# Kernel tuning notes

Hardware: AMD Instinct MI355X
Metric: run time of the kernel (lower is better)

## Reference

```python
import jax, jax.numpy as jnp
import numpy as np

NEG_SLOPE = 0.2
NUM_GRAPHS = 64


def _gatv2_layer(x, src, dst, Wl, bl, Wr, br, att, bias, n_nodes, heads, ch):
    # lin_l (source) and lin_r (target) transforms -> [N, H, C]
    xs = (x @ Wl + bl).reshape(n_nodes, heads, ch)
    xd = (x @ Wr + br).reshape(n_nodes, heads, ch)
    s = xs[src]                                   # [E, H, C] gathered source feats
    e = jax.nn.leaky_relu(s + xd[dst], NEG_SLOPE)  # GATv2: leaky_relu BEFORE att dot
    score = jnp.einsum('ehc,hc->eh', e, att)       # [E, H]
    # segment softmax over edges sharing the same target node
    smax = jax.ops.segment_max(score, dst, num_segments=n_nodes)
    ex = jnp.exp(score - smax[dst])
    denom = jax.ops.segment_sum(ex, dst, num_segments=n_nodes)
    alpha = ex / denom[dst]                        # [E, H]
    out = jax.ops.segment_sum(alpha[:, :, None] * s, dst, num_segments=n_nodes)
    return out.reshape(n_nodes, heads * ch) + bias


def setup_inputs() -> dict:
    key = jax.random.key(0)
    ks = jax.random.split(key, 20)
    N, E, F = 50000, 800000, 128
    H, C = 4, 64
    G = NUM_GRAPHS
    sc = 0.05
    inp = {
        'x': jax.random.normal(ks[0], (N, F), jnp.float32),
        'edge_index': jax.random.randint(ks[1], (2, E), 0, N, jnp.int64 if jax.config.read('jax_enable_x64') else jnp.int32).astype(jnp.int32),
        'batch': jnp.sort(jax.random.randint(ks[2], (N,), 0, G)).astype(jnp.int32),
        'W_l1': jax.random.normal(ks[3], (F, H * C)) * sc,
        'b_l1': jax.random.normal(ks[4], (H * C,)) * sc,
        'W_r1': jax.random.normal(ks[5], (F, H * C)) * sc,
        'b_r1': jax.random.normal(ks[6], (H * C,)) * sc,
        'att1': jax.random.normal(ks[7], (H, C)) * sc,
        'bias1': jax.random.normal(ks[8], (H * C,)) * sc,
        'W_l2': jax.random.normal(ks[9], (H * C, C)) * sc,
        'b_l2': jax.random.normal(ks[10], (C,)) * sc,
        'W_r2': jax.random.normal(ks[11], (H * C, C)) * sc,
        'b_r2': jax.random.normal(ks[12], (C,)) * sc,
        'att2': jax.random.normal(ks[13], (1, C)) * sc,
        'bias2': jax.random.normal(ks[14], (C,)) * sc,
        'W_lin': jax.random.normal(ks[15], (C, 1)) * sc,
        'b_lin': jax.random.normal(ks[16], (1,)) * sc,
    }
    return inp


def reference(x, edge_index, batch, W_l1, b_l1, W_r1, b_r1, att1, bias1,
              W_l2, b_l2, W_r2, b_r2, att2, bias2, W_lin, b_lin):
    N = x.shape[0]
    # PyG GATv2Conv adds self-loops by default
    loops = jnp.arange(N, dtype=edge_index.dtype)
    src = jnp.concatenate([edge_index[0], loops])
    dst = jnp.concatenate([edge_index[1], loops])

    h = _gatv2_layer(x, src, dst, W_l1, b_l1, W_r1, b_r1, att1, bias1, N, 4, 64)
    h = jax.nn.relu(h)  # dropout=identity (eval), norm=Identity
    h = _gatv2_layer(h, src, dst, W_l2, b_l2, W_r2, b_r2, att2, bias2, N, 1, 64)

    # global mean pool over graphs
    sums = jax.ops.segment_sum(h, batch, num_segments=NUM_GRAPHS)
    counts = jax.ops.segment_sum(jnp.ones((N,), h.dtype), batch, num_segments=NUM_GRAPHS)
    pooled = sums / jnp.maximum(counts, 1.0)[:, None]  # [G, 64]
    return pooled @ W_lin + b_lin                      # [G, 1]
```

## Files before the change

kernel.cpp:

```cpp
#include <hip/hip_runtime.h>
#include <hip/hip_bf16.h>
#include <math.h>

typedef __attribute__((ext_vector_type(8))) short short8;
typedef __attribute__((ext_vector_type(4))) float floatx4;
typedef __attribute__((ext_vector_type(2))) float f32x2;

#define ATT_SCALE 0.865617024533378f
#define C_ABS 0.6666666666667f
#define PCLAMP 86.5f

__device__ __forceinline__ float bf2f(unsigned short u) {
  union { unsigned int i; float f; } v; v.i = ((unsigned int)u) << 16; return v.f;
}
__device__ __forceinline__ unsigned short f2bf(float f) {
  union { float f; unsigned int u; } v; v.f = f;
  unsigned int r = (v.u + 0x7fffu + ((v.u >> 16) & 1u)) >> 16;
  return (unsigned short)r;
}
__device__ __forceinline__ int imin(int a, int b) { return a < b ? a : b; }
__device__ __forceinline__ int iclamp(int v, int lo, int hi) {
  return v < lo ? lo : (v > hi ? hi : v);
}
__device__ __forceinline__ float uasf(unsigned int u) {
// ... 142 lines not shown
  }
  if (i < N) {
    int ex = sm[tid] - v + boff;
    rowptr[i] = ex;
    cursor[i] = ex;
    if (i == N - 1) rowptr[N] = ex + v;
  }
}

template <int K, int CT, int RT>
__device__ __forceinline__ void gemm2r_body(
    int bx, int by, int tid,
    const unsigned short* __restrict__ A,
    const unsigned short* __restrict__ BTl, const unsigned short* __restrict__ BTr,
    const unsigned short* __restrict__ bl, const unsigned short* __restrict__ br,
    unsigned short* __restrict__ outl, unsigned short* __restrict__ outr,
    int Nrows, int M) {
  constexpr int KI = K / 32;
  int lane = tid & 63;
  int wave = tid >> 6;
  int r = lane & 15, q = lane >> 4;
  int col0 = by * (4 * CT * 16) + wave * (CT * 16);
  int row0 = bx * (16 * RT);
  short8 Bl[KI][CT], Br[KI][CT];
#pragma unroll
  for (int t = 0; t < CT; ++t) {
    const unsigned short* bpl = BTl + (size_t)(col0 + t * 16 + r) * K + q * 8;
    const unsigned short* bpr = BTr + (size_t)(col0 + t * 16 + r) * K + q * 8;
#pragma unroll
    for (int k = 0; k < KI; ++k) {
      Bl[k][t] = *reinterpret_cast<const short8*>(bpl + k * 32);
      Br[k][t] = *reinterpret_cast<const short8*>(bpr + k * 32);
    }
  }
  float bvl[CT], bvr[CT];
#pragma unroll
  for (int t = 0; t < CT; ++t) {
    bvl[t] = bf2f(bl[col0 + t * 16 + r]);
    bvr[t] = bf2f(br[col0 + t * 16 + r]);
  }
  short8 a[KI], an[KI];
  {
    int ar0 = imin(row0 + r, Nrows - 1);
    const unsigned short* Ap = A + (size_t)ar0 * K + q * 8;
#pragma unroll
    for (int k = 0; k < KI; ++k) a[k] = *reinterpret_cast<const short8*>(Ap + k * 32);
  }
  for (int rt = 0; rt < RT; ++rt) {
    if (rt + 1 < RT) {
      int arn = imin(row0 + (rt + 1) * 16 + r, Nrows - 1);
      const unsigned short* Apn = A + (size_t)arn * K + q * 8;
#pragma unroll
      for (int k = 0; k < KI; ++k) an[k] = *reinterpret_cast<const short8*>(Apn + k * 32);
    }
    floatx4 accl[CT], accr[CT];
#pragma unroll
    for (int t = 0; t < CT; ++t) {
      accl[t] = (floatx4){0.f, 0.f, 0.f, 0.f};
      accr[t] = (floatx4){0.f, 0.f, 0.f, 0.f};
    }
#pragma unroll
    for (int k = 0; k < KI; ++k) {
#pragma unroll
      for (int t = 0; t < CT; ++t) {
        accl[t] = __builtin_amdgcn_mfma_f32_16x16x32_bf16(a[k], Bl[k][t], accl[t], 0, 0, 0);
        accr[t] = __builtin_amdgcn_mfma_f32_16x16x32_bf16(a[k], Br[k][t], accr[t], 0, 0, 0);
      }
    }
#pragma unroll
    for (int t = 0; t < CT; ++t) {
      int col = col0 + t * 16 + r;
#pragma unroll
      for (int rr = 0; rr < 4; ++rr) {
        int row = row0 + rt * 16 + q * 4 + rr;
        if (row < Nrows) {
          outl[(size_t)row * M + col] = f2bf(accl[t][rr] + bvl[t]);
          outr[(size_t)row * M + col] = f2bf(accr[t][rr] + bvr[t]);
        }
      }
    }
#pragma unroll
    for (int k = 0; k < KI; ++k) a[k] = an[k];
  }
}

__global__ __launch_bounds__(256) void k_phase1(
    const unsigned short* __restrict__ A0, const unsigned short* __restrict__ A1,
    const int* __restrict__ dflag,
    const unsigned short* __restrict__ BTl, const unsigned short* __restrict__ BTr,
    const unsigned short* __restrict__ bl, const unsigned short* __restrict__ br,
    unsigned short* __restrict__ outl, unsigned short* __restrict__ outr,
    int Nrows, int M, int nG, int nS,
    const int* __restrict__ esrc, const int* __restrict__ edst,
    const int* __restrict__ rowptr, int* cursor, int* colx, int E, int N) {
  int b = blockIdx.x;
  int m2 = 2 * imin(nG, nS);
  bool isG;
  int idx;
  if (b < m2) { isG = (b & 1) == 0; idx = b >> 1; }
  else        { isG = nG > nS;      idx = imin(nG, nS) + (b - m2); }
  if (isG) {
    const unsigned short* A = dflag[0] ? A1 : A0;
    gemm2r_body<128, 2, 8>(idx >> 1, idx & 1, threadIdx.x, A, BTl, BTr, bl, br,
                           outl, outr, Nrows, M);
    return;
  }
  int ET = E + N;
  int base = idx * 1024 + threadIdx.x;
#pragma unroll
  for (int k = 0; k < 4; ++k) {
    int e = base + k * 256;
    if (e < ET) {
      if (e < E) {
        int s = iclamp(esrc[e], 0, N - 1), d = iclamp(edst[e], 0, N - 1);
        int pos = atomicAdd(&cursor[d], 1);
        colx[iclamp(pos, 0, ET - 1)] = s;
      } else {
        int i = e - E;
        colx[rowptr[i + 1] - 1] = i;
      }
    }
  }
}

__global__ __launch_bounds__(256) void k_gemm2r_l2(
    const unsigned short* __restrict__ A,
    const unsigned short* __restrict__ BTl, const unsigned short* __restrict__ BTr,
    const unsigned short* __restrict__ bl, const unsigned short* __restrict__ br,
    unsigned short* __restrict__ outl, unsigned short* __restrict__ outr,
    int Nrows, int M) {
  gemm2r_body<256, 1, 4>(blockIdx.x, 0, threadIdx.x, A, BTl, BTr, bl, br,
                         outl, outr, Nrows, M);
}

#define EDGE_P(U, V01, V23, P)                                                \
  V01 = (f32x2){uasf(U.x << 16), uasf(U.x & 0xffff0000u)};                    \
  V23 = (f32x2){uasf(U.y << 16), uasf(U.y & 0xffff0000u)};                    \
  {                                                                           \
    f32x2 q01 = a01 * V01 + ad01;                                             \
    f32x2 q23 = a23 * V23 + ad23;                                             \
    f32x2 t01 = c01 * absv2(q01) + q01;                                       \
    f32x2 t23 = c23 * absv2(q23) + q23;                                       \
    f32x2 sv = t01 + t23;                                                     \
    P = sv[0] + sv[1];                                                        \
  }

#define EDGE_ACC(W, V01, V23)                                                 \
  {                                                                           \
    f32x2 wv = {W, W};                                                        \
    o01 = wv * V01 + o01;                                                     \
    o23 = wv * V23 + o23;                                                     \
  }

__global__ __launch_bounds__(256) void k_agg_h4(
    const int* __restrict__ rowptr, const int* __restrict__ colx,
    const unsigned short* __restrict__ xs, const unsigned short* __restrict__ xd,
    const float* __restrict__ atts, const unsigned short* __restrict__ bias,
    unsigned short* __restrict__ hout, int N) {
  int lane = threadIdx.x & 63;
  int dst = (blockIdx.x * 256 + threadIdx.x) >> 6;
  if (dst >= N) return;
  int off = lane << 2;
  unsigned int off2 = (unsigned int)off * 2;
  const char* xsb = (const char*)xs;
  floatx4 av = *reinterpret_cast<const floatx4*>(atts + off);
  ushort4 du = *reinterpret_cast<const ushort4*>(xd + (size_t)dst * 256 + off);
  f32x2 a01 = {av[0], av[1]}, a23 = {av[2], av[3]};
  f32x2 dd01 = {bf2f(du.x), bf2f(du.y)}, dd23 = {bf2f(du.z), bf2f(du.w)};
  f32x2 ad01 = a01 * dd01, ad23 = a23 * dd23;
  f32x2 c01 = {copysignf(C_ABS, av[0]), copysignf(C_ABS, av[1])};
  f32x2 c23 = {copysignf(C_ABS, av[2]), copysignf(C_ABS, av[3])};
  float l = 0.f;
  f32x2 o01 = {0.f, 0.f}, o23 = {0.f, 0.f};
  int beg = __builtin_amdgcn_readfirstlane(rowptr[dst]);
  int end = __builtin_amdgcn_readfirstlane(rowptr[dst + 1]);
  int p0 = colx[beg], p1 = colx[beg + 1], p2 = colx[beg + 2], p3 = colx[beg + 3];
  uint2 ua = *(const uint2*)(xsb + (((unsigned)p0 << 9) + off2));
  uint2 ub = *(const uint2*)(xsb + (((unsigned)p1 << 9) + off2));
  uint2 uc = *(const uint2*)(xsb + (((unsigned)p2 << 9) + off2));
  uint2 ud = *(const uint2*)(xsb + (((unsigned)p3 << 9) + off2));
  int q0 = 0, q1 = 0, q2 = 0, q3 = 0;
  if (beg + 4 < end) {
    q0 = colx[beg + 4]; q1 = colx[beg + 5]; q2 = colx[beg + 6]; q3 = colx[beg + 7];
  }
  for (int e = beg; e < end; e += 4) {
    uint2 na = ua, nb = ub, nc = uc, nd = ud;
    if (e + 4 < end) {
      na = *(const uint2*)(xsb + (((unsigned)q0 << 9) + off2));
      nb = *(const uint2*)(xsb + (((unsigned)q1 << 9) + off2));
      nc = *(const uint2*)(xsb + (((unsigned)q2 << 9) + off2));
      nd = *(const uint2*)(xsb + (((unsigned)q3 << 9) + off2));
    }
    if (e + 8 < end) {
      q0 = colx[e + 8]; q1 = colx[e + 9]; q2 = colx[e + 10]; q3 = colx[e + 11];
    }
    f32x2 va01, va23, vb01, vb23, vc01, vc23, vd01, vd23;
    float pa, pb, pc, pd;
    EDGE_P(ua, va01, va23, pa)
    EDGE_P(ub, vb01, vb23, pb)
    EDGE_P(uc, vc01, vc23, pc)
    EDGE_P(ud, vd01, vd23, pd)
    pa = sum16(pa); pb = sum16(pb); pc = sum16(pc); pd = sum16(pd);
    pa = fminf(pa, PCLAMP);
    pb = (e + 1 < end) ? fminf(pb, PCLAMP) : -INFINITY;
    pc = (e + 2 < end) ? fminf(pc, PCLAMP) : -INFINITY;
    pd = (e + 3 < end) ? fminf(pd, PCLAMP) : -INFINITY;
    float wa = exp2fast(pa), wb = exp2fast(pb);
    float wc = exp2fast(pc), wd = exp2fast(pd);
    l += (wa + wb) + (wc + wd);
    EDGE_ACC(wa, va01, va23)
    EDGE_ACC(wb, vb01, vb23)
    EDGE_ACC(wc, vc01, vc23)
    EDGE_ACC(wd, vd01, vd23)
    ua = na; ub = nb; uc = nc; ud = nd;
  }
  float rl = 1.0f / l;
  ushort4 bu = *reinterpret_cast<const ushort4*>(bias + off);
  ushort4 res;
  res.x = f2bf(fmaxf(fmaf(o01[0], rl, bf2f(bu.x)), 0.f));
  res.y = f2bf(fmaxf(fmaf(o01[1], rl, bf2f(bu.y)), 0.f));
  res.z = f2bf(fmaxf(fmaf(o23[0], rl, bf2f(bu.z)), 0.f));
  res.w = f2bf(fmaxf(fmaf(o23[1], rl, bf2f(bu.w)), 0.f));
  *reinterpret_cast<ushort4*>(hout + (size_t)dst * 256 + off) = res;
}

__global__ __launch_bounds__(256) void k_agg_h1(
    const int* __restrict__ rowptr, const int* __restrict__ colx,
    const unsigned short* __restrict__ xs, const unsigned short* __restrict__ xd,
    const float* __restrict__ atts, const unsigned short* __restrict__ bias,
    float* __restrict__ hout, int N) {
  int lane = threadIdx.x & 63;
  int wid = (blockIdx.x * 256 + threadIdx.x) >> 6;
  int g = lane >> 4, sl = lane & 15;
  int dst = wid * 4 + g;
  bool valid = dst < N;
  int dsafe = valid ? dst : 0;
  int cb = sl << 2;
  unsigned int cb2 = (unsigned int)cb * 2;
  const char* xsb = (const char*)xs;
  floatx4 av = *reinterpret_cast<const floatx4*>(atts + cb);
  ushort4 du = *reinterpret_cast<const ushort4*>(xd + (size_t)dsafe * 64 + cb);
  f32x2 a01 = {av[0], av[1]}, a23 = {av[2], av[3]};
  f32x2 dd01 = {bf2f(du.x), bf2f(du.y)}, dd23 = {bf2f(du.z), bf2f(du.w)};
  f32x2 ad01 = a01 * dd01, ad23 = a23 * dd23;
  f32x2 c01 = {copysignf(C_ABS, av[0]), copysignf(C_ABS, av[1])};
  f32x2 c23 = {copysignf(C_ABS, av[2]), copysignf(C_ABS, av[3])};
  float l = 0.f;
  f32x2 o01 = {0.f, 0.f}, o23 = {0.f, 0.f};
  int beg = valid ? rowptr[dst] : 0;
  int end = valid ? rowptr[dst + 1] : 0;
  if (end > beg) {
    int p0 = colx[beg], p1 = colx[beg + 1], p2 = colx[beg + 2], p3 = colx[beg + 3];
    uint2 ua = *(const uint2*)(xsb + (((unsigned)p0 << 7) + cb2));
    uint2 ub = *(const uint2*)(xsb + (((unsigned)p1 << 7) + cb2));
    uint2 uc = *(const uint2*)(xsb + (((unsigned)p2 << 7) + cb2));
    uint2 ud = *(const uint2*)(xsb + (((unsigned)p3 << 7) + cb2));
    int q0 = 0, q1 = 0, q2 = 0, q3 = 0;
    if (beg + 4 < end) {
      q0 = colx[beg + 4]; q1 = colx[beg + 5]; q2 = colx[beg + 6]; q3 = colx[beg + 7];
    }
    for (int e = beg; e < end; e += 4) {
      uint2 na = ua, nb = ub, nc = uc, nd = ud;
      if (e + 4 < end) {
        na = *(const uint2*)(xsb + (((unsigned)q0 << 7) + cb2));
        nb = *(const uint2*)(xsb + (((unsigned)q1 << 7) + cb2));
        nc = *(const uint2*)(xsb + (((unsigned)q2 << 7) + cb2));
        nd = *(const uint2*)(xsb + (((unsigned)q3 << 7) + cb2));
      }
      if (e + 8 < end) {
        q0 = colx[e + 8]; q1 = colx[e + 9]; q2 = colx[e + 10]; q3 = colx[e + 11];
      }
      f32x2 va01, va23, vb01, vb23, vc01, vc23, vd01, vd23;
      float pa, pb, pc, pd;
      EDGE_P(ua, va01, va23, pa)
      EDGE_P(ub, vb01, vb23, pb)
      EDGE_P(uc, vc01, vc23, pc)
      EDGE_P(ud, vd01, vd23, pd)
      pa = sum16(pa); pb = sum16(pb); pc = sum16(pc); pd = sum16(pd);
      pa = fminf(pa, PCLAMP);
      pb = (e + 1 < end) ? fminf(pb, PCLAMP) : -INFINITY;
      pc = (e + 2 < end) ? fminf(pc, PCLAMP) : -INFINITY;
      pd = (e + 3 < end) ? fminf(pd, PCLAMP) : -INFINITY;
      float wa = exp2fast(pa), wb = exp2fast(pb);
      float wc = exp2fast(pc), wd = exp2fast(pd);
      l += (wa + wb) + (wc + wd);
      EDGE_ACC(wa, va01, va23)
      EDGE_ACC(wb, vb01, vb23)
      EDGE_ACC(wc, vc01, vc23)
      EDGE_ACC(wd, vd01, vd23)
      ua = na; ub = nb; uc = nc; ud = nd;
    }
  }
  if (valid) {
    float rl = 1.0f / l;
    ushort4 bu = *reinterpret_cast<const ushort4*>(bias + cb);
    floatx4 res;
    res[0] = fmaf(o01[0], rl, bf2f(bu.x));
    res[1] = fmaf(o01[1], rl, bf2f(bu.y));
    res[2] = fmaf(o23[0], rl, bf2f(bu.z));
    res[3] = fmaf(o23[1], rl, bf2f(bu.w));
    *reinterpret_cast<floatx4*>(hout + (size_t)dst * 64 + cb) = res;
  }
}

__global__ __launch_bounds__(256) void k_pool(const float* __restrict__ h2,
                                              const int* __restrict__ batch,
                                              float* pool, int* cnt, int N) {
  int lane = threadIdx.x & 63;
  int wid = (blockIdx.x * 256 + threadIdx.x) >> 6;
  int n0 = wid * 32;
  if (n0 >= N) return;
  int nend = imin(n0 + 32, N);
  float acc = 0.f;
  int c = 0;
  int gcur = iclamp(batch[n0], 0, 63);
  for (int n = n0; n < nend; ++n) {
    int gg = iclamp(batch[n], 0, 63);
    if (gg != gcur) {
      atomicAdd(&pool[gcur * 64 + lane], acc);
      if (lane == 0) atomicAdd(&cnt[gcur], c);
      acc = 0.f; c = 0; gcur = gg;
    }
    acc += h2[(size_t)n * 64 + lane];
    c++;
  }
  atomicAdd(&pool[gcur * 64 + lane], acc);
  if (lane == 0) atomicAdd(&cnt[gcur], c);
}

__global__ void k_final(const float* __restrict__ pool, const int* __restrict__ cnt,
                        const unsigned short* __restrict__ Wlinc,
                        const unsigned short* __restrict__ blinc,
                        float* __restrict__ out) {
  int g = threadIdx.x;
  if (g >= 64) return;
  float inv = 1.f / fmaxf((float)cnt[g], 1.f);
  float s = 0.f;
  for (int c = 0; c < 64; ++c) s += pool[g * 64 + c] * bf2f(Wlinc[c]);
  out[g] = fmaf(s, inv, bf2f(blinc[0]));
}

extern "C" void kernel_launch(void* const* d_in, const int* in_sizes, int n_in,
                              void* d_out, int out_size, void* d_ws, size_t ws_size,
                              hipStream_t stream) {
  const void* x     = d_in[0];
  const int*  ei    = (const int*)d_in[1];
  const int*  batch = (const int*)d_in[2];
  const void* Wl1 = d_in[3];  const void* bl1 = d_in[4];
  const void* Wr1 = d_in[5];  const void* br1 = d_in[6];
  const void* att1 = d_in[7]; const void* bias1 = d_in[8];
  const void* Wl2 = d_in[9];  const void* bl2 = d_in[10];
  const void* Wr2 = d_in[11]; const void* br2 = d_in[12];
  const void* att2 = d_in[13]; const void* bias2 = d_in[14];
  const void* Wlin = d_in[15]; const void* blin = d_in[16];
  float* out = (float*)d_out;

  const int F = 128, HC = 256, C2 = 64;
  int N = in_sizes[0] / F;
  int E = in_sizes[1] / 2;
  int ET = E + N;
  const int* esrc = ei;
  const int* edst = ei + E;

  char* w = (char*)d_ws;
  auto alloc = [&](size_t bytes) {
    char* p = w;
    w += (bytes + 255) & ~(size_t)255;
    return p;
  };
  int* dflag  = (int*)alloc(4);
  int* rowptr = (int*)alloc((size_t)(N + 1) * 4);
  int* cursor = (int*)alloc((size_t)N * 4);
  int* bsum   = (int*)alloc(1024 * 4);
  int* colx   = (int*)alloc((size_t)(ET + 16) * 4);
  unsigned short* smallc = (unsigned short*)alloc(4096);
  float* att1s = (float*)alloc(256 * 4);
  float* att2s = (float*)alloc(64 * 4);
  unsigned short* Wl1T = (unsigned short*)alloc((size_t)F * HC * 2);
  unsigned short* Wr1T = (unsigned short*)alloc((size_t)F * HC * 2);
  unsigned short* Wl2T = (unsigned short*)alloc((size_t)HC * C2 * 2);
  unsigned short* Wr2T = (unsigned short*)alloc((size_t)HC * C2 * 2);
  int* deg    = (int*)alloc((size_t)N * 4);
  float* pool = (float*)alloc(64 * 64 * 4);
  int* cnt    = (int*)alloc(64 * 4);
  unsigned short* xs1  = (unsigned short*)alloc((size_t)N * HC * 2);
  unsigned short* xd1  = (unsigned short*)alloc((size_t)N * HC * 2);
  unsigned short* h1   = (unsigned short*)alloc((size_t)N * HC * 2);
  size_t required = (size_t)(w - (char*)d_ws);
  size_t zlen = (size_t)((char*)cnt + 256 - (char*)deg);

  unsigned short* x_c = h1;
  unsigned short* xs2 = xs1;
  unsigned short* xd2 = xs1 + (size_t)N * C2;
  float*          h2  = (float*)xd1;

  unsigned short* bl1c   = smallc + 0;
  unsigned short* br1c   = smallc + 256;
  unsigned short* att1c  = smallc + 512;
  unsigned short* bias1c = smallc + 768;
  unsigned short* bl2c   = smallc + 1024;
  unsigned short* br2c   = smallc + 1088;
  unsigned short* att2c  = smallc + 1152;
  unsigned short* bias2c = smallc + 1216;
  unsigned short* Wlinc  = smallc + 1280;
  unsigned short* blinc  = smallc + 1344;

  if (ws_size < required) {
    k_sentinel<<<1, 64, 0, stream>>>(out, 1000.f + (float)(ws_size >> 20));
    return;
  }

  hipMemsetAsync(deg, 0, zlen, stream);

  CvtSegs segs;
  const void* ssrc[10] = {bl1, br1, att1, bias1, bl2, br2, att2, bias2, Wlin, blin};
  unsigned short* sdst[10] = {bl1c, br1c, att1c, bias1c, bl2c, br2c, att2c, bias2c, Wlinc, blinc};
  int slen[10] = {256, 256, 256, 256, 64, 64, 64, 64, 64, 1};
  for (int i = 0; i < 10; ++i) { segs.src[i] = ssrc[i]; segs.dst[i] = sdst[i]; segs.len[i] = slen[i]; }
  int n8 = N * F / 8;
  int nCvt8 = (n8 + 255) / 256;
  int nTransB = (2 * F * HC + 2 * HC * C2 + 255) / 256;
  int nHist = (E + 1023) / 1024;
  k_prep<<<nCvt8 + 10 + nTransB + nHist, 256, 0, stream>>>(
      x, x_c, n8, segs, Wl1, Wr1, Wl2, Wr2, Wl1T, Wr1T, Wl2T, Wr2T,
      edst, deg, E, N, dflag, colx, ET, att1s, att2s, nCvt8, nTransB);

  int nb = (N + 1023) / 1024;
  k_scan1<<<nb, 1024, 0, stream>>>(deg, bsum, N);
  k_scan3<<<nb, 1024, 0, stream>>>(deg, bsum, rowptr, cursor, N);

  int nG = ((N + 127) / 128) * 2;
  int nS = (ET + 1023) / 1024;
  k_phase1<<<nG + nS, 256, 0, stream>>>(
      (const unsigned short*)x, x_c, dflag, Wl1T, Wr1T, bl1c, br1c, xs1, xd1,
      N, HC, nG, nS, esrc, edst, rowptr, cursor, colx, E, N);

  k_agg_h4<<<(N + 3) / 4, 256, 0, stream>>>(rowptr, colx, xs1, xd1, att1s, bias1c, h1, N);

  k_gemm2r_l2<<<(N + 63) / 64, 256, 0, stream>>>(h1, Wl2T, Wr2T, bl2c, br2c, xs2, xd2, N, C2);
  k_agg_h1<<<(N + 15) / 16, 256, 0, stream>>>(rowptr, colx, xs2, xd2, att2s, bias2c, h2, N);

  int pw = (N + 31) / 32;
  k_pool<<<(pw + 3) / 4, 256, 0, stream>>>(h2, batch, pool, cnt, N);
  k_final<<<1, 64, 0, stream>>>(pool, cnt, Wlinc, blinc, out);
}
```

Baseline: 334.1 us.

## Process two destination rows per wave with prologue gathers issued up front

Each wave in both aggregation kernels now handles two destination nodes instead of one. The first-stage neighbor gathers for both rows are issued before either row's loop starts, so the second row's latency is hidden behind the first row's work. The per-iteration bounds checks on prefetch gathers and colx index loads are removed, which relies on padded colx and valid index reads past the row end. This halves the wave count and reduces occupancy, and it adds register pressure and serial work per wave.

```diff
diff --git a/kernel.cpp b/kernel.cpp
--- a/kernel.cpp
+++ b/kernel.cpp
@@ -318,48 +318,18 @@
     o23 = wv * V23 + o23;                                                     \
   }
 
-__global__ __launch_bounds__(256) void k_agg_h4(
-    const int* __restrict__ rowptr, const int* __restrict__ colx,
-    const unsigned short* __restrict__ xs, const unsigned short* __restrict__ xd,
-    const float* __restrict__ atts, const unsigned short* __restrict__ bias,
-    unsigned short* __restrict__ hout, int N) {
-  int lane = threadIdx.x & 63;
-  int dst = (blockIdx.x * 256 + threadIdx.x) >> 6;
-  if (dst >= N) return;
-  int off = lane << 2;
-  unsigned int off2 = (unsigned int)off * 2;
-  const char* xsb = (const char*)xs;
-  floatx4 av = *reinterpret_cast<const floatx4*>(atts + off);
-  ushort4 du = *reinterpret_cast<const ushort4*>(xd + (size_t)dst * 256 + off);
-  f32x2 a01 = {av[0], av[1]}, a23 = {av[2], av[3]};
-  f32x2 dd01 = {bf2f(du.x), bf2f(du.y)}, dd23 = {bf2f(du.z), bf2f(du.w)};
-  f32x2 ad01 = a01 * dd01, ad23 = a23 * dd23;
-  f32x2 c01 = {copysignf(C_ABS, av[0]), copysignf(C_ABS, av[1])};
-  f32x2 c23 = {copysignf(C_ABS, av[2]), copysignf(C_ABS, av[3])};
-  float l = 0.f;
-  f32x2 o01 = {0.f, 0.f}, o23 = {0.f, 0.f};
-  int beg = __builtin_amdgcn_readfirstlane(rowptr[dst]);
-  int end = __builtin_amdgcn_readfirstlane(rowptr[dst + 1]);
-  int p0 = colx[beg], p1 = colx[beg + 1], p2 = colx[beg + 2], p3 = colx[beg + 3];
-  uint2 ua = *(const uint2*)(xsb + (((unsigned)p0 << 9) + off2));
-  uint2 ub = *(const uint2*)(xsb + (((unsigned)p1 << 9) + off2));
-  uint2 uc = *(const uint2*)(xsb + (((unsigned)p2 << 9) + off2));
-  uint2 ud = *(const uint2*)(xsb + (((unsigned)p3 << 9) + off2));
-  int q0 = 0, q1 = 0, q2 = 0, q3 = 0;
-  if (beg + 4 < end) {
-    q0 = colx[beg + 4]; q1 = colx[beg + 5]; q2 = colx[beg + 6]; q3 = colx[beg + 7];
-  }
+template <int LOG_ROWB>
+__device__ __forceinline__ void agg_row(
+    const char* __restrict__ xsb, const int* __restrict__ colx, unsigned off2,
+    int beg, int end,
+    f32x2 a01, f32x2 a23, f32x2 c01, f32x2 c23, f32x2 ad01, f32x2 ad23,
+    uint2 ua, uint2 ub, uint2 uc, uint2 ud,
+    int q0, int q1, int q2, int q3,
+    float& l, f32x2& o01, f32x2& o23) {
+#define GATH(p) (*(const uint2*)(xsb + (((unsigned)(p) << LOG_ROWB) + off2)))
   for (int e = beg; e < end; e += 4) {
-    uint2 na = ua, nb = ub, nc = uc, nd = ud;
-    if (e + 4 < end) {
-      na = *(const uint2*)(xsb + (((unsigned)q0 << 9) + off2));
-      nb = *(const uint2*)(xsb + (((unsigned)q1 << 9) + off2));
-      nc = *(const uint2*)(xsb + (((unsigned)q2 << 9) + off2));
-      nd = *(const uint2*)(xsb + (((unsigned)q3 << 9) + off2));
-    }
-    if (e + 8 < end) {
-      q0 = colx[e + 8]; q1 = colx[e + 9]; q2 = colx[e + 10]; q3 = colx[e + 11];
-    }
+    uint2 na = GATH(q0), nb = GATH(q1), nc = GATH(q2), nd = GATH(q3);
+    q0 = colx[e + 8]; q1 = colx[e + 9]; q2 = colx[e + 10]; q3 = colx[e + 11];
     f32x2 va01, va23, vb01, vb23, vc01, vc23, vd01, vd23;
     float pa, pb, pc, pd;
     EDGE_P(ua, va01, va23, pa)
@@ -380,14 +350,73 @@
     EDGE_ACC(wd, vd01, vd23)
     ua = na; ub = nb; uc = nc; ud = nd;
   }
-  float rl = 1.0f / l;
+#undef GATH
+}
+
+__global__ __launch_bounds__(256) void k_agg_h4(
+    const int* __restrict__ rowptr, const int* __restrict__ colx,
+    const unsigned short* __restrict__ xs, const unsigned short* __restrict__ xd,
+    const float* __restrict__ atts, const unsigned short* __restrict__ bias,
+    unsigned short* __restrict__ hout, int N) {
+  int lane = threadIdx.x & 63;
+  int wid = (blockIdx.x * 256 + threadIdx.x) >> 6;
+  int d0 = wid * 2;
+  if (d0 >= N) return;
+  int d1 = d0 + 1;
+  bool v1 = d1 < N;
+  int off = lane << 2;
+  unsigned int off2 = (unsigned int)off * 2;
+  const char* xsb = (const char*)xs;
+  int beg0 = __builtin_amdgcn_readfirstlane(rowptr[d0]);
+  int end0 = __builtin_amdgcn_readfirstlane(rowptr[d0 + 1]);
+  int end1 = v1 ? __builtin_amdgcn_readfirstlane(rowptr[d1 + 1]) : end0;
+  int beg1 = end0;
+#define GATH4(p) (*(const uint2*)(xsb + (((unsigned)(p) << 9) + off2)))
+  int p0 = colx[beg0], p1 = colx[beg0 + 1], p2 = colx[beg0 + 2], p3 = colx[beg0 + 3];
+  uint2 uA0 = GATH4(p0), uA1 = GATH4(p1), uA2 = GATH4(p2), uA3 = GATH4(p3);
+  int qa0 = colx[beg0 + 4], qa1 = colx[beg0 + 5], qa2 = colx[beg0 + 6], qa3 = colx[beg0 + 7];
+  int r0 = colx[beg1], r1 = colx[beg1 + 1], r2 = colx[beg1 + 2], r3 = colx[beg1 + 3];
+  uint2 uB0 = GATH4(r0), uB1 = GATH4(r1), uB2 = GATH4(r2), uB3 = GATH4(r3);
+  int qb0 = colx[beg1 + 4], qb1 = colx[beg1 + 5], qb2 = colx[beg1 + 6], qb3 = colx[beg1 + 7];
+#undef GATH4
+  floatx4 av = *reinterpret_cast<const floatx4*>(atts + off);
+  f32x2 a01 = {av[0], av[1]}, a23 = {av[2], av[3]};
+  f32x2 c01 = {copysignf(C_ABS, av[0]), copysignf(C_ABS, av[1])};
+  f32x2 c23 = {copysignf(C_ABS, av[2]), copysignf(C_ABS, av[3])};
+  ushort4 du0 = *reinterpret_cast<const ushort4*>(xd + (size_t)d0 * 256 + off);
+  ushort4 du1 = *reinterpret_cast<const ushort4*>(xd + (size_t)(v1 ? d1 : d0) * 256 + off);
   ushort4 bu = *reinterpret_cast<const ushort4*>(bias + off);
-  ushort4 res;
-  res.x = f2bf(fmaxf(fmaf(o01[0], rl, bf2f(bu.x)), 0.f));
-  res.y = f2bf(fmaxf(fmaf(o01[1], rl, bf2f(bu.y)), 0.f));
-  res.z = f2bf(fmaxf(fmaf(o23[0], rl, bf2f(bu.z)), 0.f));
-  res.w = f2bf(fmaxf(fmaf(o23[1], rl, bf2f(bu.w)), 0.f));
-  *reinterpret_cast<ushort4*>(hout + (size_t)dst * 256 + off) = res;
+  float b0f = bf2f(bu.x), b1f = bf2f(bu.y), b2f = bf2f(bu.z), b3f = bf2f(bu.w);
+  {
+    f32x2 dd01 = {bf2f(du0.x), bf2f(du0.y)}, dd23 = {bf2f(du0.z), bf2f(du0.w)};
+    f32x2 ad01 = a01 * dd01, ad23 = a23 * dd23;
+    float l = 0.f;
+    f32x2 o01 = {0.f, 0.f}, o23 = {0.f, 0.f};
+    agg_row<9>(xsb, colx, off2, beg0, end0, a01, a23, c01, c23, ad01, ad23,
+               uA0, uA1, uA2, uA3, qa0, qa1, qa2, qa3, l, o01, o23);
+    float rl = 1.0f / l;
+    ushort4 res;
+    res.x = f2bf(fmaxf(fmaf(o01[0], rl, b0f), 0.f));
+    res.y = f2bf(fmaxf(fmaf(o01[1], rl, b1f), 0.f));
+    res.z = f2bf(fmaxf(fmaf(o23[0], rl, b2f), 0.f));
+    res.w = f2bf(fmaxf(fmaf(o23[1], rl, b3f), 0.f));
+    *reinterpret_cast<ushort4*>(hout + (size_t)d0 * 256 + off) = res;
+  }
+  if (v1) {
+    f32x2 dd01 = {bf2f(du1.x), bf2f(du1.y)}, dd23 = {bf2f(du1.z), bf2f(du1.w)};
+    f32x2 ad01 = a01 * dd01, ad23 = a23 * dd23;
+    float l = 0.f;
+    f32x2 o01 = {0.f, 0.f}, o23 = {0.f, 0.f};
+    agg_row<9>(xsb, colx, off2, beg1, end1, a01, a23, c01, c23, ad01, ad23,
+               uB0, uB1, uB2, uB3, qb0, qb1, qb2, qb3, l, o01, o23);
+    float rl = 1.0f / l;
+    ushort4 res;
+    res.x = f2bf(fmaxf(fmaf(o01[0], rl, b0f), 0.f));
+    res.y = f2bf(fmaxf(fmaf(o01[1], rl, b1f), 0.f));
+    res.z = f2bf(fmaxf(fmaf(o23[0], rl, b2f), 0.f));
+    res.w = f2bf(fmaxf(fmaf(o23[1], rl, b3f), 0.f));
+    *reinterpret_cast<ushort4*>(hout + (size_t)d1 * 256 + off) = res;
+  }
 }
 
 __global__ __launch_bounds__(256) void k_agg_h1(
@@ -398,74 +427,66 @@
   int lane = threadIdx.x & 63;
   int wid = (blockIdx.x * 256 + threadIdx.x) >> 6;
   int g = lane >> 4, sl = lane & 15;
-  int dst = wid * 4 + g;
-  bool valid = dst < N;
-  int dsafe = valid ? dst : 0;
+  int d0 = wid * 8 + g;
+  int d1 = d0 + 4;
+  bool v0 = d0 < N, v1 = d1 < N;
+  int ds0 = v0 ? d0 : 0, ds1 = v1 ? d1 : 0;
   int cb = sl << 2;
   unsigned int cb2 = (unsigned int)cb * 2;
   const char* xsb = (const char*)xs;
+  int beg0 = v0 ? rowptr[d0] : 0;
+  int end0 = v0 ? rowptr[d0 + 1] : 0;
+  int beg1 = v1 ? rowptr[d1] : 0;
+  int end1 = v1 ? rowptr[d1 + 1] : 0;
+#define GATH1(p) (*(const uint2*)(xsb + (((unsigned)(p) << 7) + cb2)))
+  int p0 = colx[beg0], p1 = colx[beg0 + 1], p2 = colx[beg0 + 2], p3 = colx[beg0 + 3];
+  uint2 uA0 = GATH1(p0), uA1 = GATH1(p1), uA2 = GATH1(p2), uA3 = GATH1(p3);
+  int qa0 = colx[beg0 + 4], qa1 = colx[beg0 + 5], qa2 = colx[beg0 + 6], qa3 = colx[beg0 + 7];
+  int r0 = colx[beg1], r1 = colx[beg1 + 1], r2 = colx[beg1 + 2], r3 = colx[beg1 + 3];
+  uint2 uB0 = GATH1(r0), uB1 = GATH1(r1), uB2 = GATH1(r2), uB3 = GATH1(r3);
+  int qb0 = colx[beg1 + 4], qb1 = colx[beg1 + 5], qb2 = colx[beg1 + 6], qb3 = colx[beg1 + 7];
+#undef GATH1
   floatx4 av = *reinterpret_cast<const floatx4*>(atts + cb);
-  ushort4 du = *reinterpret_cast<const ushort4*>(xd + (size_t)dsafe * 64 + cb);
   f32x2 a01 = {av[0], av[1]}, a23 = {av[2], av[3]};
-  f32x2 dd01 = {bf2f(du.x), bf2f(du.y)}, dd23 = {bf2f(du.z), bf2f(du.w)};
-  f32x2 ad01 = a01 * dd01, ad23 = a23 * dd23;
   f32x2 c01 = {copysignf(C_ABS, av[0]), copysignf(C_ABS, av[1])};
   f32x2 c23 = {copysignf(C_ABS, av[2]), copysignf(C_ABS, av[3])};
-  float l = 0.f;
-  f32x2 o01 = {0.f, 0.f}, o23 = {0.f, 0.f};
-  int beg = valid ? rowptr[dst] : 0;
-  int end = valid ? rowptr[dst + 1] : 0;
-  if (end > beg) {
-    int p0 = colx[beg], p1 = colx[beg + 1], p2 = colx[beg + 2], p3 = colx[beg + 3];
-    uint2 ua = *(const uint2*)(xsb + (((unsigned)p0 << 7) + cb2));
-    uint2 ub = *(const uint2*)(xsb + (((unsigned)p1 << 7) + cb2));
-    uint2 uc = *(const uint2*)(xsb + (((unsigned)p2 << 7) + cb2));
-    uint2 ud = *(const uint2*)(xsb + (((unsigned)p3 << 7) + cb2));
-    int q0 = 0, q1 = 0, q2 = 0, q3 = 0;
-    if (beg + 4 < end) {
-      q0 = colx[beg + 4]; q1 = colx[beg + 5]; q2 = colx[beg + 6]; q3 = colx[beg + 7];
-    }
-    for (int e = beg; e < end; e += 4) {
-      uint2 na = ua, nb = ub, nc = uc, nd = ud;
-      if (e + 4 < end) {
-        na = *(const uint2*)(xsb + (((unsigned)q0 << 7) + cb2));
-        nb = *(const uint2*)(xsb + (((unsigned)q1 << 7) + cb2));
-        nc = *(const uint2*)(xsb + (((unsigned)q2 << 7) + cb2));
-        nd = *(const uint2*)(xsb + (((unsigned)q3 << 7) + cb2));
-      }
-      if (e + 8 < end) {
-        q0 = colx[e + 8]; q1 = colx[e + 9]; q2 = colx[e + 10]; q3 = colx[e + 11];
-      }
-      f32x2 va01, va23, vb01, vb23, vc01, vc23, vd01, vd23;
-      float pa, pb, pc, pd;
-      EDGE_P(ua, va01, va23, pa)
-      EDGE_P(ub, vb01, vb23, pb)
-      EDGE_P(uc, vc01, vc23, pc)
-      EDGE_P(ud, vd01, vd23, pd)
-      pa = sum16(pa); pb = sum16(pb); pc = sum16(pc); pd = sum16(pd);
-      pa = fminf(pa, PCLAMP);
-      pb = (e + 1 < end) ? fminf(pb, PCLAMP) : -INFINITY;
-      pc = (e + 2 < end) ? fminf(pc, PCLAMP) : -INFINITY;
-      pd = (e + 3 < end) ? fminf(pd, PCLAMP) : -INFINITY;
-      float wa = exp2fast(pa), wb = exp2fast(pb);
-      float wc = exp2fast(pc), wd = exp2fast(pd);
-      l += (wa + wb) + (wc + wd);
-      EDGE_ACC(wa, va01, va23)
-      EDGE_ACC(wb, vb01, vb23)
-      EDGE_ACC(wc, vc01, vc23)
-      EDGE_ACC(wd, vd01, vd23)
-      ua = na; ub = nb; uc = nc; ud = nd;
-    }
-  }
-  if (valid) {
-    float rl = 1.0f / l;
-    ushort4 bu = *reinterpret_cast<const ushort4*>(bias + cb);
-    floatx4 res;
-    res[0] = fmaf(o01[0], rl, bf2f(bu.x));
-    res[1] = fmaf(o01[1], rl, bf2f(bu.y));
-    res[2] = fmaf(o23[0], rl, bf2f(bu.z));
-    res[3] = fmaf(o23[1], rl, bf2f(bu.w));
-    *reinterpret_cast<floatx4*>(hout + (size_t)dst * 64 + cb) = res;
+  ushort4 du0 = *reinterpret_cast<const ushort4*>(xd + (size_t)ds0 * 64 + cb);
+  ushort4 du1 = *reinterpret_cast<const ushort4*>(xd + (size_t)ds1 * 64 + cb);
+  ushort4 bu = *reinterpret_cast<const ushort4*>(bias + cb);
+  float b0f = bf2f(bu.x), b1f = bf2f(bu.y), b2f = bf2f(bu.z), b3f = bf2f(bu.w);
+  {
+    f32x2 dd01 = {bf2f(du0.x), bf2f(du0.y)}, dd23 = {bf2f(du0.z), bf2f(du0.w)};
+    f32x2 ad01 = a01 * dd01, ad23 = a23 * dd23;
+    float l = 0.f;
+    f32x2 o01 = {0.f, 0.f}, o23 = {0.f, 0.f};
+    agg_row<7>(xsb, colx, cb2, beg0, end0, a01, a23, c01, c23, ad01, ad23,
+               uA0, uA1, uA2, uA3, qa0, qa1, qa2, qa3, l, o01, o23);
+    if (v0) {
+      float rl = 1.0f / l;
+      floatx4 res;
+      res[0] = fmaf(o01[0], rl, b0f);
+      res[1] = fmaf(o01[1], rl, b1f);
+      res[2] = fmaf(o23[0], rl, b2f);
+      res[3] = fmaf(o23[1], rl, b3f);
+      *reinterpret_cast<floatx4*>(hout + (size_t)d0 * 64 + cb) = res;
+    }
+  }
+  {
+    f32x2 dd01 = {bf2f(du1.x), bf2f(du1.y)}, dd23 = {bf2f(du1.z), bf2f(du1.w)};
+    f32x2 ad01 = a01 * dd01, ad23 = a23 * dd23;
+    float l = 0.f;
+    f32x2 o01 = {0.f, 0.f}, o23 = {0.f, 0.f};
+    agg_row<7>(xsb, colx, cb2, beg1, end1, a01, a23, c01, c23, ad01, ad23,
+               uB0, uB1, uB2, uB3, qb0, qb1, qb2, qb3, l, o01, o23);
+    if (v1) {
+      float rl = 1.0f / l;
+      floatx4 res;
+      res[0] = fmaf(o01[0], rl, b0f);
+      res[1] = fmaf(o01[1], rl, b1f);
+      res[2] = fmaf(o23[0], rl, b2f);
+      res[3] = fmaf(o23[1], rl, b3f);
+      *reinterpret_cast<floatx4*>(hout + (size_t)d1 * 64 + cb) = res;
+    }
   }
 }
 
@@ -601,10 +622,12 @@
       (const unsigned short*)x, x_c, dflag, Wl1T, Wr1T, bl1c, br1c, xs1, xd1,
       N, HC, nG, nS, esrc, edst, rowptr, cursor, colx, E, N);
 
-  k_agg_h4<<<(N + 3) / 4, 256, 0, stream>>>(rowptr, colx, xs1, xd1, att1s, bias1c, h1, N);
+  int nw4 = (N + 1) / 2;
+  k_agg_h4<<<(nw4 + 3) / 4, 256, 0, stream>>>(rowptr, colx, xs1, xd1, att1s, bias1c, h1, N);
 
   k_gemm2r_l2<<<(N + 63) / 64, 256, 0, stream>>>(h1, Wl2T, Wr2T, bl2c, br2c, xs2, xd2, N, C2);
-  k_agg_h1<<<(N + 15) / 16, 256, 0, stream>>>(rowptr, colx, xs2, xd2, att2s, bias2c, h2, N);
+  int nw1 = (N + 7) / 8;
+  k_agg_h1<<<(nw1 + 3) / 4, 256, 0, stream>>>(rowptr, colx, xs2, xd2, att2s, bias2c, h2, N);
 
   int pw = (N + 31) / 32;
   k_pool<<<(pw + 3) / 4, 256, 0, stream>>>(h2, batch, pool, cnt, N);
```

Measured after the change: 345.2 us. +3.3%, slower.

## Use persistent atomic work-queue for layer-1 aggregation and rework layer-2 scoring math

Applied to the files above, without the earlier changes.

Layer-1 aggregation becomes a persistent kernel with 2048 blocks. Each wavefront repeatedly claims pairs of destination nodes through an atomic counter held in workspace, which is zeroed along with the existing cleared range. This is meant to cut launch and tail overhead and balance uneven degrees. Layer-2 aggregation now reads the raw bf16 attention vector, writes the leaky-relu score as scalar FMAs (0.6q + 0.4|q|), and uses __expf instead of prescaled exp2. It also drops the packed-float2 math, which may change instruction count and numeric behaviour slightly.

```diff
diff --git a/kernel.cpp b/kernel.cpp
--- a/kernel.cpp
+++ b/kernel.cpp
@@ -322,78 +322,92 @@
     const int* __restrict__ rowptr, const int* __restrict__ colx,
     const unsigned short* __restrict__ xs, const unsigned short* __restrict__ xd,
     const float* __restrict__ atts, const unsigned short* __restrict__ bias,
-    unsigned short* __restrict__ hout, int N) {
+    unsigned short* __restrict__ hout, int* __restrict__ wsc, int N) {
   int lane = threadIdx.x & 63;
-  int dst = (blockIdx.x * 256 + threadIdx.x) >> 6;
-  if (dst >= N) return;
   int off = lane << 2;
   unsigned int off2 = (unsigned int)off * 2;
   const char* xsb = (const char*)xs;
   floatx4 av = *reinterpret_cast<const floatx4*>(atts + off);
-  ushort4 du = *reinterpret_cast<const ushort4*>(xd + (size_t)dst * 256 + off);
   f32x2 a01 = {av[0], av[1]}, a23 = {av[2], av[3]};
-  f32x2 dd01 = {bf2f(du.x), bf2f(du.y)}, dd23 = {bf2f(du.z), bf2f(du.w)};
-  f32x2 ad01 = a01 * dd01, ad23 = a23 * dd23;
   f32x2 c01 = {copysignf(C_ABS, av[0]), copysignf(C_ABS, av[1])};
   f32x2 c23 = {copysignf(C_ABS, av[2]), copysignf(C_ABS, av[3])};
-  float l = 0.f;
-  f32x2 o01 = {0.f, 0.f}, o23 = {0.f, 0.f};
-  int beg = __builtin_amdgcn_readfirstlane(rowptr[dst]);
-  int end = __builtin_amdgcn_readfirstlane(rowptr[dst + 1]);
-  int p0 = colx[beg], p1 = colx[beg + 1], p2 = colx[beg + 2], p3 = colx[beg + 3];
-  uint2 ua = *(const uint2*)(xsb + (((unsigned)p0 << 9) + off2));
-  uint2 ub = *(const uint2*)(xsb + (((unsigned)p1 << 9) + off2));
-  uint2 uc = *(const uint2*)(xsb + (((unsigned)p2 << 9) + off2));
-  uint2 ud = *(const uint2*)(xsb + (((unsigned)p3 << 9) + off2));
-  int q0 = 0, q1 = 0, q2 = 0, q3 = 0;
-  if (beg + 4 < end) {
-    q0 = colx[beg + 4]; q1 = colx[beg + 5]; q2 = colx[beg + 6]; q3 = colx[beg + 7];
-  }
-  for (int e = beg; e < end; e += 4) {
-    uint2 na = ua, nb = ub, nc = uc, nd = ud;
-    if (e + 4 < end) {
-      na = *(const uint2*)(xsb + (((unsigned)q0 << 9) + off2));
-      nb = *(const uint2*)(xsb + (((unsigned)q1 << 9) + off2));
-      nc = *(const uint2*)(xsb + (((unsigned)q2 << 9) + off2));
-      nd = *(const uint2*)(xsb + (((unsigned)q3 << 9) + off2));
-    }
-    if (e + 8 < end) {
-      q0 = colx[e + 8]; q1 = colx[e + 9]; q2 = colx[e + 10]; q3 = colx[e + 11];
-    }
-    f32x2 va01, va23, vb01, vb23, vc01, vc23, vd01, vd23;
-    float pa, pb, pc, pd;
-    EDGE_P(ua, va01, va23, pa)
-    EDGE_P(ub, vb01, vb23, pb)
-    EDGE_P(uc, vc01, vc23, pc)
-    EDGE_P(ud, vd01, vd23, pd)
-    pa = sum16(pa); pb = sum16(pb); pc = sum16(pc); pd = sum16(pd);
-    pa = fminf(pa, PCLAMP);
-    pb = (e + 1 < end) ? fminf(pb, PCLAMP) : -INFINITY;
-    pc = (e + 2 < end) ? fminf(pc, PCLAMP) : -INFINITY;
-    pd = (e + 3 < end) ? fminf(pd, PCLAMP) : -INFINITY;
-    float wa = exp2fast(pa), wb = exp2fast(pb);
-    float wc = exp2fast(pc), wd = exp2fast(pd);
-    l += (wa + wb) + (wc + wd);
-    EDGE_ACC(wa, va01, va23)
-    EDGE_ACC(wb, vb01, vb23)
-    EDGE_ACC(wc, vc01, vc23)
-    EDGE_ACC(wd, vd01, vd23)
-    ua = na; ub = nb; uc = nc; ud = nd;
-  }
-  float rl = 1.0f / l;
   ushort4 bu = *reinterpret_cast<const ushort4*>(bias + off);
-  ushort4 res;
-  res.x = f2bf(fmaxf(fmaf(o01[0], rl, bf2f(bu.x)), 0.f));
-  res.y = f2bf(fmaxf(fmaf(o01[1], rl, bf2f(bu.y)), 0.f));
-  res.z = f2bf(fmaxf(fmaf(o23[0], rl, bf2f(bu.z)), 0.f));
-  res.w = f2bf(fmaxf(fmaf(o23[1], rl, bf2f(bu.w)), 0.f));
-  *reinterpret_cast<ushort4*>(hout + (size_t)dst * 256 + off) = res;
-}
+  float b0f = bf2f(bu.x), b1f = bf2f(bu.y), b2f = bf2f(bu.z), b3f = bf2f(bu.w);
+#define GATH(p) (*(const uint2*)(xsb + (((unsigned)(p) << 9) + off2)))
+  for (;;) {
+    int bpop;
+    if (lane == 0) bpop = atomicAdd(wsc, 2);
+    bpop = __shfl(bpop, 0);
+    if (bpop >= N) break;
+    int dlim = imin(bpop + 2, N);
+    for (int dst = bpop; dst < dlim; ++dst) {
+      int beg = __builtin_amdgcn_readfirstlane(rowptr[dst]);
+      int end = __builtin_amdgcn_readfirstlane(rowptr[dst + 1]);
+      int p0 = colx[beg], p1 = colx[beg + 1], p2 = colx[beg + 2], p3 = colx[beg + 3];
+      uint2 ua = GATH(p0), ub = GATH(p1), uc = GATH(p2), ud = GATH(p3);
+      int q0 = 0, q1 = 0, q2 = 0, q3 = 0;
+      if (beg + 4 < end) {
+        q0 = colx[beg + 4]; q1 = colx[beg + 5]; q2 = colx[beg + 6]; q3 = colx[beg + 7];
+      }
+      ushort4 du = *reinterpret_cast<const ushort4*>(xd + (size_t)dst * 256 + off);
+      f32x2 dd01 = {bf2f(du.x), bf2f(du.y)}, dd23 = {bf2f(du.z), bf2f(du.w)};
+      f32x2 ad01 = a01 * dd01, ad23 = a23 * dd23;
+      float l = 0.f;
+      f32x2 o01 = {0.f, 0.f}, o23 = {0.f, 0.f};
+      for (int e = beg; e < end; e += 4) {
+        uint2 na = ua, nb = ub, nc = uc, nd = ud;
+        if (e + 4 < end) {
+          na = GATH(q0); nb = GATH(q1); nc = GATH(q2); nd = GATH(q3);
+        }
+        if (e + 8 < end) {
+          q0 = colx[e + 8]; q1 = colx[e + 9]; q2 = colx[e + 10]; q3 = colx[e + 11];
+        }
+        f32x2 va01, va23, vb01, vb23, vc01, vc23, vd01, vd23;
+        float pa, pb, pc, pd;
+        EDGE_P(ua, va01, va23, pa)
+        EDGE_P(ub, vb01, vb23, pb)
+        EDGE_P(uc, vc01, vc23, pc)
+        EDGE_P(ud, vd01, vd23, pd)
+        pa = sum16(pa); pb = sum16(pb); pc = sum16(pc); pd = sum16(pd);
+        pa = fminf(pa, PCLAMP);
+        pb = (e + 1 < end) ? fminf(pb, PCLAMP) : -INFINITY;
+        pc = (e + 2 < end) ? fminf(pc, PCLAMP) : -INFINITY;
+        pd = (e + 3 < end) ? fminf(pd, PCLAMP) : -INFINITY;
+        float wa = exp2fast(pa), wb = exp2fast(pb);
+        float wc = exp2fast(pc), wd = exp2fast(pd);
+        l += (wa + wb) + (wc + wd);
+        EDGE_ACC(wa, va01, va23)
+        EDGE_ACC(wb, vb01, vb23)
+        EDGE_ACC(wc, vc01, vc23)
+        EDGE_ACC(wd, vd01, vd23)
+        ua = na; ub = nb; uc = nc; ud = nd;
+      }
+      float rl = 1.0f / l;
+      ushort4 res;
+      res.x = f2bf(fmaxf(fmaf(o01[0], rl, b0f), 0.f));
+      res.y = f2bf(fmaxf(fmaf(o01[1], rl, b1f), 0.f));
+      res.z = f2bf(fmaxf(fmaf(o23[0], rl, b2f), 0.f));
+      res.w = f2bf(fmaxf(fmaf(o23[1], rl, b3f), 0.f));
+      *reinterpret_cast<ushort4*>(hout + (size_t)dst * 256 + off) = res;
+    }
+  }
+#undef GATH
+}
+
+#define UNPACK2(u, v0, v1, v2, v3)          \
+  v0 = uasf(u.x << 16); v1 = uasf(u.x & 0xffff0000u); \
+  v2 = uasf(u.y << 16); v3 = uasf(u.y & 0xffff0000u);
+
+#define SCORE(q0, q1, q2, q3, p)                             \
+  p = q0 * 0.6f;                                             \
+  p = fmaf(q1, 0.6f, p); p = fmaf(q2, 0.6f, p); p = fmaf(q3, 0.6f, p); \
+  p = fmaf(c0, fabsf(q0), p); p = fmaf(c1, fabsf(q1), p);    \
+  p = fmaf(c2, fabsf(q2), p); p = fmaf(c3, fabsf(q3), p);
 
 __global__ __launch_bounds__(256) void k_agg_h1(
     const int* __restrict__ rowptr, const int* __restrict__ colx,
     const unsigned short* __restrict__ xs, const unsigned short* __restrict__ xd,
-    const float* __restrict__ atts, const unsigned short* __restrict__ bias,
+    const unsigned short* __restrict__ att, const unsigned short* __restrict__ bias,
     float* __restrict__ hout, int N) {
   int lane = threadIdx.x & 63;
   int wid = (blockIdx.x * 256 + threadIdx.x) >> 6;
@@ -404,15 +418,14 @@
   int cb = sl << 2;
   unsigned int cb2 = (unsigned int)cb * 2;
   const char* xsb = (const char*)xs;
-  floatx4 av = *reinterpret_cast<const floatx4*>(atts + cb);
+  ushort4 au = *reinterpret_cast<const ushort4*>(att + cb);
   ushort4 du = *reinterpret_cast<const ushort4*>(xd + (size_t)dsafe * 64 + cb);
-  f32x2 a01 = {av[0], av[1]}, a23 = {av[2], av[3]};
-  f32x2 dd01 = {bf2f(du.x), bf2f(du.y)}, dd23 = {bf2f(du.z), bf2f(du.w)};
-  f32x2 ad01 = a01 * dd01, ad23 = a23 * dd23;
-  f32x2 c01 = {copysignf(C_ABS, av[0]), copysignf(C_ABS, av[1])};
-  f32x2 c23 = {copysignf(C_ABS, av[2]), copysignf(C_ABS, av[3])};
-  float l = 0.f;
-  f32x2 o01 = {0.f, 0.f}, o23 = {0.f, 0.f};
+  float a0 = bf2f(au.x), a1 = bf2f(au.y), a2 = bf2f(au.z), a3 = bf2f(au.w);
+  float d0 = bf2f(du.x), d1 = bf2f(du.y), d2 = bf2f(du.z), d3 = bf2f(du.w);
+  float ad0 = a0 * d0, ad1 = a1 * d1, ad2 = a2 * d2, ad3 = a3 * d3;
+  float c0 = copysignf(0.4f, a0), c1 = copysignf(0.4f, a1);
+  float c2 = copysignf(0.4f, a2), c3 = copysignf(0.4f, a3);
+  float l = 0.f, o0 = 0.f, o1 = 0.f, o2 = 0.f, o3 = 0.f;
   int beg = valid ? rowptr[dst] : 0;
   int end = valid ? rowptr[dst + 1] : 0;
   if (end > beg) {
@@ -436,24 +449,40 @@
       if (e + 8 < end) {
         q0 = colx[e + 8]; q1 = colx[e + 9]; q2 = colx[e + 10]; q3 = colx[e + 11];
       }
-      f32x2 va01, va23, vb01, vb23, vc01, vc23, vd01, vd23;
+      float va0, va1, va2, va3, vb0, vb1, vb2, vb3;
+      float vc0, vc1, vc2, vc3, vd0, vd1, vd2, vd3;
+      UNPACK2(ua, va0, va1, va2, va3)
+      UNPACK2(ub, vb0, vb1, vb2, vb3)
+      UNPACK2(uc, vc0, vc1, vc2, vc3)
+      UNPACK2(ud, vd0, vd1, vd2, vd3)
+      float qa0 = fmaf(a0, va0, ad0), qa1 = fmaf(a1, va1, ad1);
+      float qa2 = fmaf(a2, va2, ad2), qa3 = fmaf(a3, va3, ad3);
+      float qb0 = fmaf(a0, vb0, ad0), qb1 = fmaf(a1, vb1, ad1);
+      float qb2 = fmaf(a2, vb2, ad2), qb3 = fmaf(a3, vb3, ad3);
+      float qc0 = fmaf(a0, vc0, ad0), qc1 = fmaf(a1, vc1, ad1);
+      float qc2 = fmaf(a2, vc2, ad2), qc3 = fmaf(a3, vc3, ad3);
+      float qd0 = fmaf(a0, vd0, ad0), qd1 = fmaf(a1, vd1, ad1);
+      float qd2 = fmaf(a2, vd2, ad2), qd3 = fmaf(a3, vd3, ad3);
       float pa, pb, pc, pd;
-      EDGE_P(ua, va01, va23, pa)
-      EDGE_P(ub, vb01, vb23, pb)
-      EDGE_P(uc, vc01, vc23, pc)
-      EDGE_P(ud, vd01, vd23, pd)
+      SCORE(qa0, qa1, qa2, qa3, pa)
+      SCORE(qb0, qb1, qb2, qb3, pb)
+      SCORE(qc0, qc1, qc2, qc3, pc)
+      SCORE(qd0, qd1, qd2, qd3, pd)
       pa = sum16(pa); pb = sum16(pb); pc = sum16(pc); pd = sum16(pd);
-      pa = fminf(pa, PCLAMP);
-      pb = (e + 1 < end) ? fminf(pb, PCLAMP) : -INFINITY;
-      pc = (e + 2 < end) ? fminf(pc, PCLAMP) : -INFINITY;
-      pd = (e + 3 < end) ? fminf(pd, PCLAMP) : -INFINITY;
-      float wa = exp2fast(pa), wb = exp2fast(pb);
-      float wc = exp2fast(pc), wd = exp2fast(pd);
+      pa = fminf(pa, 60.f);
+      pb = (e + 1 < end) ? fminf(pb, 60.f) : -INFINITY;
+      pc = (e + 2 < end) ? fminf(pc, 60.f) : -INFINITY;
+      pd = (e + 3 < end) ? fminf(pd, 60.f) : -INFINITY;
+      float wa = __expf(pa), wb = __expf(pb), wc = __expf(pc), wd = __expf(pd);
       l += (wa + wb) + (wc + wd);
-      EDGE_ACC(wa, va01, va23)
-      EDGE_ACC(wb, vb01, vb23)
-      EDGE_ACC(wc, vc01, vc23)
-      EDGE_ACC(wd, vd01, vd23)
+      o0 = fmaf(wa, va0, o0); o0 = fmaf(wb, vb0, o0);
+      o0 = fmaf(wc, vc0, o0); o0 = fmaf(wd, vd0, o0);
+      o1 = fmaf(wa, va1, o1); o1 = fmaf(wb, vb1, o1);
+      o1 = fmaf(wc, vc1, o1); o1 = fmaf(wd, vd1, o1);
+      o2 = fmaf(wa, va2, o2); o2 = fmaf(wb, vb2, o2);
+      o2 = fmaf(wc, vc2, o2); o2 = fmaf(wd, vd2, o2);
+      o3 = fmaf(wa, va3, o3); o3 = fmaf(wb, vb3, o3);
+      o3 = fmaf(wc, vc3, o3); o3 = fmaf(wd, vd3, o3);
       ua = na; ub = nb; uc = nc; ud = nd;
     }
   }
@@ -461,10 +490,10 @@
     float rl = 1.0f / l;
     ushort4 bu = *reinterpret_cast<const ushort4*>(bias + cb);
     floatx4 res;
-    res[0] = fmaf(o01[0], rl, bf2f(bu.x));
-    res[1] = fmaf(o01[1], rl, bf2f(bu.y));
-    res[2] = fmaf(o23[0], rl, bf2f(bu.z));
-    res[3] = fmaf(o23[1], rl, bf2f(bu.w));
+    res[0] = fmaf(o0, rl, bf2f(bu.x));
+    res[1] = fmaf(o1, rl, bf2f(bu.y));
+    res[2] = fmaf(o2, rl, bf2f(bu.z));
+    res[3] = fmaf(o3, rl, bf2f(bu.w));
     *reinterpret_cast<floatx4*>(hout + (size_t)dst * 64 + cb) = res;
   }
 }
@@ -549,11 +578,12 @@
   int* deg    = (int*)alloc((size_t)N * 4);
   float* pool = (float*)alloc(64 * 64 * 4);
   int* cnt    = (int*)alloc(64 * 4);
+  int* wsc    = (int*)alloc(4);
   unsigned short* xs1  = (unsigned short*)alloc((size_t)N * HC * 2);
   unsigned short* xd1  = (unsigned short*)alloc((size_t)N * HC * 2);
   unsigned short* h1   = (unsigned short*)alloc((size_t)N * HC * 2);
   size_t required = (size_t)(w - (char*)d_ws);
-  size_t zlen = (size_t)((char*)cnt + 256 - (char*)deg);
+  size_t zlen = (size_t)((char*)wsc + 256 - (char*)deg);
 
   unsigned short* x_c = h1;
   unsigned short* xs2 = xs1;
@@ -601,10 +631,10 @@
       (const unsigned short*)x, x_c, dflag, Wl1T, Wr1T, bl1c, br1c, xs1, xd1,
       N, HC, nG, nS, esrc, edst, rowptr, cursor, colx, E, N);
 
-  k_agg_h4<<<(N + 3) / 4, 256, 0, stream>>>(rowptr, colx, xs1, xd1, att1s, bias1c, h1, N);
+  k_agg_h4<<<2048, 256, 0, stream>>>(rowptr, colx, xs1, xd1, att1s, bias1c, h1, wsc, N);
 
   k_gemm2r_l2<<<(N + 63) / 64, 256, 0, stream>>>(h1, Wl2T, Wr2T, bl2c, br2c, xs2, xd2, N, C2);
-  k_agg_h1<<<(N + 15) / 16, 256, 0, stream>>>(rowptr, colx, xs2, xd2, att2s, bias2c, h2, N);
+  k_agg_h1<<<(N + 15) / 16, 256, 0, stream>>>(rowptr, colx, xs2, xd2, att2c, bias2c, h2, N);
 
   int pw = (N + 31) / 32;
   k_pool<<<(pw + 3) / 4, 256, 0, stream>>>(h2, batch, pool, cnt, N);
```

Result: slower. 658.6 us (+97.2%).
